# Optimization experiments

Measured on AMD Instinct MI355X. Metric: run time of the kernel, lower is better.

Reference implementation:

```python
import jax, jax.numpy as jnp
import numpy as np

D_STATE = 16
LOW_RANK = 6


def _scan_fwd(t):
    # 'interwave' scan: (B, stream, signal, C, H, W) -> (stream, B, C, H*W*signal)
    st, B, C = t.shape[1], t.shape[0], t.shape[3]
    t = jnp.transpose(t, (1, 0, 3, 4, 5, 2))  # stream,B,C,H,W,signal
    return t.reshape(st, B, C, -1)


def _scan_bwd(t, sg, H, W):
    # inverse 'interwave': (stream, B, C, H*W*sg) -> (B, stream, sg, C, H, W)
    st, B, C, _ = t.shape
    t = t.reshape(st, B, C, H, W, sg)
    return jnp.transpose(t, (1, 0, 5, 2, 3, 4))


def _layernorm(t, w, b):
    # LayerNorm over last (channel) axis, eps=1e-5 (torch default)
    mu = t.mean(-1, keepdims=True)
    var = t.var(-1, keepdims=True)
    return (t - mu) * jax.lax.rsqrt(var + 1e-5) * w + b


def reference(x, x_proj_weight, dt_projs_weight, dt_projs_bias, A_logs, Ds, norm_weight, norm_bias):
    B, S, C, H, W = x.shape
    stream = S + 1
    G = 4 * stream            # scan_direction * stream groups
    N = D_STATE
    R = LOW_RANK
    L = S * H * W             # unistream_length
    i = jnp.arange(S - 1)
    j = jnp.arange(S)

    # ---- CommDiffSS2DScan (cross-scan) ----
    x_comm_0 = _scan_fwd(x[:, None])                                  # (1,B,C,L)
    x_comm_1 = _scan_fwd(jnp.swapaxes(x, -1, -2)[:, None])
    x_dif = x[:, :, None] - x[:, None, :]                             # (B,S,S,C,H,W)
    x_dif = x_dif.at[:, i, i].set(x_dif[:, i, S - 1])
    x_dif = x_dif.at[:, :, S - 1].set(x)
    x_diff_0 = _scan_fwd(x_dif)                                       # (S,B,C,L)
    x_diff_1 = _scan_fwd(jnp.swapaxes(x_dif, -1, -2))
    xs0 = jnp.concatenate([x_diff_0, x_comm_0], 0)                    # (stream,B,C,L)
    xs1 = jnp.concatenate([x_diff_1, x_comm_1], 0)
    xs = jnp.stack([xs0, xs1, xs0[..., ::-1], xs1[..., ::-1]], 0)     # (4,stream,B,C,L)
    xs = jnp.transpose(xs, (2, 0, 1, 3, 4))                           # (B,4,stream,C,L)

    # ---- input-dependent projections ----
    x_dbl = jnp.einsum('bkscl,kspc->bkspl', xs, x_proj_weight)        # (B,4,stream,R+2N,L)
    dts, Bs, Cs = jnp.split(x_dbl, [R, R + N], axis=3)
    dts = jnp.einsum('bksrl,kscr->bkscl', dts, dt_projs_weight)       # (B,4,stream,C,L)

    u = xs.reshape(B, G, C, L)
    delta = jax.nn.softplus(dts.reshape(B, G, C, L) + dt_projs_bias.reshape(G, C)[None, :, :, None])
    A = -jnp.exp(A_logs).reshape(G, C, N)
    Bm = Bs.reshape(B, G, N, L)
    Cm = Cs.reshape(B, G, N, L)

    # ---- selective scan along L ----
    def step(h, inp):
        u_, d_, b_, c_ = inp                                          # (B,G,C),(B,G,C),(B,G,N),(B,G,N)
        h = h * jnp.exp(d_[..., None] * A) + (d_ * u_)[..., None] * b_[:, :, None, :]
        return h, jnp.einsum('bgcn,bgn->bgc', h, c_)

    h0 = jnp.zeros((B, G, C, N), x.dtype)
    _, ys = jax.lax.scan(step, h0, (jnp.moveaxis(u, -1, 0), jnp.moveaxis(delta, -1, 0),
                                    jnp.moveaxis(Bm, -1, 0), jnp.moveaxis(Cm, -1, 0)))
    ys = jnp.moveaxis(ys, 0, -1) + Ds.reshape(G, C)[None, :, :, None] * u  # (B,G,C,L)

    # ---- CommDiffSS2DMerge (cross-merge) ----
    ys = jnp.transpose(ys.reshape(B, 4, stream, C, L), (1, 2, 0, 3, 4))   # (4,stream,B,C,L)
    ys = ys[:2] + ys[2:, ..., ::-1]                                       # (2,stream,B,C,L)
    yd = _scan_bwd(ys[0, :S], S, H, W) + jnp.swapaxes(_scan_bwd(ys[1, :S], S, W, H), -1, -2)
    y = yd[:, :, S - 1]
    yd = yd.at[:, i, S - 1].set(yd[:, i, i])
    yd = yd.at[:, j, j].set(0.0)
    y_dif_extend = yd.sum(2)
    y_com = (_scan_bwd(ys[0, S:], S, H, W) + jnp.swapaxes(_scan_bwd(ys[1, S:], S, W, H), -1, -2)).reshape(B, S, C, H, W)

    tocl = lambda t: jnp.transpose(t, (0, 1, 3, 4, 2))  # channels-last for out_norm
    return (_layernorm(tocl(y), norm_weight, norm_bias),
            _layernorm(tocl(y_com), norm_weight, norm_bias),
            _layernorm(tocl(y_dif_extend), norm_weight, norm_bias))


def setup_inputs() -> dict:
    key = jax.random.key(0)
    ks = jax.random.split(key, 6)
    B, S, C, H, W = 4, 2, 96, 32, 32
    stream = S + 1
    G = 4 * stream
    N, R = D_STATE, LOW_RANK
    P = N + N + R
    return {
        'x': jax.random.normal(ks[0], (B, S, C, H, W), jnp.float32),
        'x_proj_weight': jax.random.normal(ks[1], (4, stream, P, C), jnp.float32) * 0.1,
        'dt_projs_weight': jax.random.normal(ks[2], (4, stream, C, R), jnp.float32) * 0.1,
        'dt_projs_bias': jax.random.uniform(ks[3], (G * C,), jnp.float32) * 0.1,
        'A_logs': jax.random.uniform(ks[4], (G * C, N), jnp.float32),
        'Ds': jax.random.normal(ks[5], (G * C,), jnp.float32) * 0.1,
        'norm_weight': jnp.ones((C,), jnp.float32),
        'norm_bias': jnp.zeros((C,), jnp.float32),
    }
```

## Files before the change

### kernel.cpp

```cpp
#include <hip/hip_runtime.h>
#include <math.h>

typedef float f4 __attribute__((ext_vector_type(4)));
typedef float f2 __attribute__((ext_vector_type(2)));

#define L_LEN 2048
#define C_DIM 96
#define N_DIM 16
#define R_DIM 6
#define G_DIM 12
#define B_DIM 4
#define NCHUNK 64
#define CLEN 32
#define BGC (B_DIM * G_DIM * C_DIM)

#define SZ_DELTA (B_DIM * G_DIM * L_LEN * C_DIM)
#define SZ_BC (B_DIM * G_DIM * N_DIM * L_LEN)
#define SZ_U6 (B_DIM * 6 * C_DIM * L_LEN)
#define SZ_Y (B_DIM * G_DIM * C_DIM * L_LEN)
#define SZ_H (BGC * NCHUNK * N_DIM)
#define SZ_S (BGC * NCHUNK)
#define SZ_X (B_DIM * 2 * C_DIM * 1024)
#define SZ_WPAD (G_DIM * 40 * C_DIM)

__device__ __forceinline__ float fexp2(float x) { return __builtin_amdgcn_exp2f(x); }

__device__ __forceinline__ float softplus_f(float x)
{
    float sp = __logf(1.f + __expf(x));
    return (x > 20.f) ? x : sp;
}

__global__ __launch_bounds__(256) void k0_xT(
    const float* __restrict__ x, float* __restrict__ xT)
{
    __shared__ float t[32][33];
    int img = blockIdx.x;
    const float* src = x + (size_t)img * 1024;
    float* dst = xT + (size_t)img * 1024;
    int tx = threadIdx.x & 31, ty = threadIdx.x >> 5;
#pragma unroll
    for (int r = 0; r < 32; r += 8) t[ty + r][tx] = src[(ty + r) * 32 + tx];
    __syncthreads();
#pragma unroll
    for (int r = 0; r < 32; r += 8) dst[(ty + r) * 32 + tx] = t[tx][ty + r];
}

__global__ __launch_bounds__(256) void k0b_padw(
    const float* __restrict__ xpw, float* __restrict__ wpad)
{
    int i = blockIdx.x * 256 + (int)threadIdx.x;
    if (i >= G_DIM * 40 * C_DIM) return;
    int g = i / (40 * C_DIM);
    int rem = i - g * 40 * C_DIM;
    int p = rem / C_DIM, c = rem - (rem / C_DIM) * C_DIM;
    wpad[i] = (p < 38) ? xpw[((size_t)g * 38 + p) * C_DIM + c] : 0.f;
}

__global__ __launch_bounds__(256) void k1_proj(
    const float* __restrict__ x, const float* __restrict__ xT,
    const float* __restrict__ wpad, const float* __restrict__ dtw,
    const float* __restrict__ dtb,
    float* __restrict__ deltaT, float* __restrict__ Bsw,
    float* __restrict__ Csw, float* __restrict__ u6T)
{
    __shared__ float Vsh[C_DIM * 68];
    __shared__ float Psh[40][68];

    int blk = blockIdx.x;
    int ltile = blk & 31;
    int bks = blk >> 5;
    int s = bks % 3;
    int k = (bks / 3) & 1;
    int b = bks / 6;
    int g = k * 3 + s;
    int gh = g + 6;
    int l0 = ltile * 64;
    int l0h = (31 - ltile) * 64;
    int bg = b * G_DIM + g;
    int bgh = b * G_DIM + gh;
    int tid = (int)threadIdx.x;

    const float* xb = (k ? xT : x) + (size_t)b * 2 * C_DIM * 1024;

#pragma unroll
    for (int j = 0; j < 6; ++j) {
        int e = tid + j * 256;
        int c = e >> 4;
        int llq = (e & 15) * 4;
        int pp = (l0 + llq) >> 1;
        f2 x0 = *(const f2*)(xb + (size_t)c * 1024 + pp);
        f2 x1 = *(const f2*)(xb + (size_t)(C_DIM + c) * 1024 + pp);
        f4 v;
        if (s == 2)      { v[0] = x0.x; v[1] = x1.x; v[2] = x0.y; v[3] = x1.y; }
        else if (s == 1) { v[0] = x1.x - x0.x; v[1] = x1.x; v[2] = x1.y - x0.y; v[3] = x1.y; }
        else             { v[0] = x0.x - x1.x; v[1] = x0.x; v[2] = x0.y - x1.y; v[3] = x0.y; }
        *(f4*)(Vsh + c * 68 + llq) = v;
    }
    __syncthreads();

    {
        size_t ub = ((size_t)(b * 6 + g) * L_LEN + l0) * C_DIM;
#pragma unroll
        for (int j = 0; j < 6; ++j) {
            int e = tid + j * 256;
            int lidx = e / 24;
            int c4 = (e - lidx * 24) * 4;
            f4 v = { Vsh[(c4 + 0) * 68 + lidx], Vsh[(c4 + 1) * 68 + lidx],
                     Vsh[(c4 + 2) * 68 + lidx], Vsh[(c4 + 3) * 68 + lidx] };
            *(f4*)(u6T + ub + (size_t)lidx * C_DIM + c4) = v;
        }
    }

    int ll = tid & 63;
    int P0 = __builtin_amdgcn_readfirstlane((tid >> 6) * 10);
    const float* wp = wpad + (size_t)g * 3840 + (size_t)P0 * C_DIM;
    const float* wph = wpad + (size_t)gh * 3840 + (size_t)P0 * C_DIM;

    float acc[10], acch[10];
#pragma unroll
    for (int p = 0; p < 10; ++p) { acc[p] = 0.f; acch[p] = 0.f; }

    for (int cb = 0; cb < C_DIM; cb += 8) {
        float vc[8], vch[8];
#pragma unroll
        for (int i = 0; i < 8; ++i) {
            vc[i] = Vsh[(cb + i) * 68 + ll];
            vch[i] = Vsh[(cb + i) * 68 + 63 - ll];
        }
#pragma unroll
        for (int p = 0; p < 10; ++p) {
#pragma unroll
            for (int q = 0; q < 2; ++q) {
                f4 w = *(const f4*)(wp + p * C_DIM + cb + q * 4);
                f4 wh = *(const f4*)(wph + p * C_DIM + cb + q * 4);
#pragma unroll
                for (int i = 0; i < 4; ++i) {
                    acc[p] = fmaf(w[i], vc[q * 4 + i], acc[p]);
                    acch[p] = fmaf(wh[i], vch[q * 4 + i], acch[p]);
                }
            }
        }
    }

#pragma unroll
    for (int gg = 0; gg < 2; ++gg) {
        __syncthreads();
#pragma unroll
        for (int p = 0; p < 10; ++p) Psh[P0 + p][ll] = gg ? acch[p] : acc[p];
        __syncthreads();
        int lb = gg ? l0h : l0;
        int bgx = gg ? bgh : bg;
        int gx = gg ? gh : g;
        int q = tid & 3, lx = tid >> 2;
        f4 bv = { Psh[6 + q * 4 + 0][lx], Psh[6 + q * 4 + 1][lx],
                  Psh[6 + q * 4 + 2][lx], Psh[6 + q * 4 + 3][lx] };
        *(f4*)(Bsw + ((size_t)bgx * L_LEN + lb + lx) * N_DIM + q * 4) = bv;
        f4 cv = { Psh[22 + q * 4 + 0][lx], Psh[22 + q * 4 + 1][lx],
                  Psh[22 + q * 4 + 2][lx], Psh[22 + q * 4 + 3][lx] };
        *(f4*)(Csw + ((size_t)bgx * L_LEN + lb + lx) * N_DIM + q * 4) = cv;

        const float* wdg = dtw + (size_t)gx * C_DIM * R_DIM;
        const float* biasg = dtb + gx * C_DIM;
        size_t db = ((size_t)bgx * L_LEN + lb) * C_DIM;
        for (int e = tid; e < 64 * C_DIM; e += 256) {
            int lidx = e / 96, c = e - (e / 96) * 96;
            float dsum = biasg[c];
#pragma unroll
            for (int r = 0; r < R_DIM; ++r) dsum = fmaf(Psh[r][lidx], wdg[c * R_DIM + r], dsum);
            deltaT[db + (size_t)lidx * C_DIM + c] = softplus_f(dsum);
        }
    }
}

__global__ __launch_bounds__(192) void k2_scanA(
    const float* __restrict__ deltaT, const float* __restrict__ Bsw,
    const float* __restrict__ u6T, const float* __restrict__ A_logs,
    float* __restrict__ hend, float* __restrict__ Sbuf)
{
    __shared__ f4 Bsh[256];
    int blk = blockIdx.x;
    int chgrp = blk & 31;
    int bg = blk >> 5;
    int g = bg % G_DIM;
    int b = bg / G_DIM;
    int tid = (int)threadIdx.x;

    const f4* Bg = (const f4*)(Bsw + ((size_t)bg * L_LEN + chgrp * 64) * N_DIM);
    for (int i = tid; i < 256; i += 192) Bsh[i] = Bg[i];
    __syncthreads();

    int chl = tid / 96;
    int c = tid % 96;
    int ch = chgrp * 2 + chl;
    int bgc = bg * C_DIM + c;
    const bool rev = (g >= 6);
    int gu = rev ? (g - 6) : g;

    float a2[N_DIM];
    {
        const f4* Ap = (const f4*)(A_logs + ((size_t)g * C_DIM + c) * N_DIM);
        f4 Av[4] = { Ap[0], Ap[1], Ap[2], Ap[3] };
#pragma unroll
        for (int n = 0; n < N_DIM; ++n)
            a2[n] = -__expf(Av[n >> 2][n & 3]) * 1.44269504f;
    }

    const int LOFF = ch * CLEN;
    const float* dp = deltaT + ((size_t)bg * L_LEN + LOFF) * C_DIM + c;
    const float* up;
    int us;
    if (rev) { up = u6T + ((size_t)(b * 6 + gu) * L_LEN + (2047 - LOFF)) * C_DIM + c; us = -C_DIM; }
    else     { up = u6T + ((size_t)(b * 6 + gu) * L_LEN + LOFF) * C_DIM + c; us = C_DIM; }

    float h[N_DIM];
#pragma unroll
    for (int n = 0; n < N_DIM; ++n) h[n] = 0.f;
    float S = 0.f;

    float dbuf[4], ubuf[4];
#pragma unroll
    for (int j = 0; j < 4; ++j) { dbuf[j] = dp[j * C_DIM]; ubuf[j] = up[j * us]; }

    for (int jj = 0; jj < CLEN; jj += 4) {
        int nx = (jj + 4 < CLEN) ? jj + 4 : jj;
        float dn[4], un[4];
#pragma unroll
        for (int j = 0; j < 4; ++j) { dn[j] = dp[(nx + j) * C_DIM]; un[j] = up[(nx + j) * us]; }
#pragma unroll
        for (int j = 0; j < 4; ++j) {
            int li = chl * CLEN + jj + j;
            float d = dbuf[j];
            S += d;
            float du = d * ubuf[j];
            const f4* Bl = Bsh + (size_t)li * 4;
            f4 Bv[4] = { Bl[0], Bl[1], Bl[2], Bl[3] };
#pragma unroll
            for (int n = 0; n < N_DIM; ++n) {
                float e = fexp2(d * a2[n]);
                h[n] = fmaf(h[n], e, du * Bv[n >> 2][n & 3]);
            }
        }
#pragma unroll
        for (int j = 0; j < 4; ++j) { dbuf[j] = dn[j]; ubuf[j] = un[j]; }
    }
    float* hp = hend + ((size_t)bgc * NCHUNK + ch) * N_DIM;
#pragma unroll
    for (int q = 0; q < 4; ++q) {
        f4 hv = { h[q * 4], h[q * 4 + 1], h[q * 4 + 2], h[q * 4 + 3] };
        *(f4*)(hp + q * 4) = hv;
    }
    Sbuf[(size_t)bgc * NCHUNK + ch] = S;
}

__global__ __launch_bounds__(256) void k2_fix(
    const float* __restrict__ Sbuf, const float* __restrict__ A_logs, float* hh)
{
    int t = blockIdx.x * 256 + (int)threadIdx.x;
    int n = t & 15;
    int bgc = t >> 4;
    int c = bgc % C_DIM;
    int g = (bgc / C_DIM) % G_DIM;
    float a2 = -__expf(A_logs[((size_t)g * C_DIM + c) * N_DIM + n]) * 1.44269504f;
    const float* Sp = Sbuf + (size_t)bgc * NCHUNK;
    float h = 0.f;
    for (int ch = 0; ch < NCHUNK; ++ch) {
        size_t idx = ((size_t)bgc * NCHUNK + ch) * N_DIM + n;
        float he = hh[idx];
        float P = fexp2(a2 * Sp[ch]);
        hh[idx] = h;
        h = fmaf(h, P, he);
    }
}

__global__ __launch_bounds__(192) void k2_scanC(
    const float* __restrict__ deltaT, const float* __restrict__ Bsw,
    const float* __restrict__ Csw, const float* __restrict__ u6T,
    const float* __restrict__ A_logs, const float* __restrict__ Ds,
    const float* __restrict__ hstart, float* __restrict__ yssT)
{
    __shared__ f4 Bsh[256];
    __shared__ f4 Csh[256];
    int blk = blockIdx.x;
    int chgrp = blk & 31;
    int bg = blk >> 5;
    int g = bg % G_DIM;
    int b = bg / G_DIM;
    int tid = (int)threadIdx.x;

    const f4* Bg = (const f4*)(Bsw + ((size_t)bg * L_LEN + chgrp * 64) * N_DIM);
    const f4* Cg = (const f4*)(Csw + ((size_t)bg * L_LEN + chgrp * 64) * N_DIM);
    for (int i = tid; i < 256; i += 192) { Bsh[i] = Bg[i]; Csh[i] = Cg[i]; }
    __syncthreads();

    int chl = tid / 96;
    int c = tid % 96;
    int ch = chgrp * 2 + chl;
    int bgc = bg * C_DIM + c;
    const bool rev = (g >= 6);
    int gu = rev ? (g - 6) : g;

    float a2[N_DIM];
    {
        const f4* Ap = (const f4*)(A_logs + ((size_t)g * C_DIM + c) * N_DIM);
        f4 Av[4] = { Ap[0], Ap[1], Ap[2], Ap[3] };
#pragma unroll
        for (int n = 0; n < N_DIM; ++n)
            a2[n] = -__expf(Av[n >> 2][n & 3]) * 1.44269504f;
    }
    float dsc = Ds[g * C_DIM + c];

    const int LOFF = ch * CLEN;
    const float* dp = deltaT + ((size_t)bg * L_LEN + LOFF) * C_DIM + c;
    const float* up;
    int us;
    if (rev) { up = u6T + ((size_t)(b * 6 + gu) * L_LEN + (2047 - LOFF)) * C_DIM + c; us = -C_DIM; }
    else     { up = u6T + ((size_t)(b * 6 + gu) * L_LEN + LOFF) * C_DIM + c; us = C_DIM; }
    float* yp = yssT + ((size_t)bg * L_LEN + LOFF) * C_DIM + c;

    float h[N_DIM];
    {
        const f4* Hp = (const f4*)(hstart + ((size_t)bgc * NCHUNK + ch) * N_DIM);
        f4 Hv[4] = { Hp[0], Hp[1], Hp[2], Hp[3] };
#pragma unroll
        for (int n = 0; n < N_DIM; ++n) h[n] = Hv[n >> 2][n & 3];
    }

    float dbuf[4], ubuf[4];
#pragma unroll
    for (int j = 0; j < 4; ++j) { dbuf[j] = dp[j * C_DIM]; ubuf[j] = up[j * us]; }

    for (int jj = 0; jj < CLEN; jj += 4) {
        int nx = (jj + 4 < CLEN) ? jj + 4 : jj;
        float dn[4], un[4];
#pragma unroll
        for (int j = 0; j < 4; ++j) { dn[j] = dp[(nx + j) * C_DIM]; un[j] = up[(nx + j) * us]; }
#pragma unroll
        for (int j = 0; j < 4; ++j) {
            int li = chl * CLEN + jj + j;
            float d = dbuf[j];
            float uu = ubuf[j];
            float du = d * uu;
            const f4* Bl = Bsh + (size_t)li * 4;
            const f4* Cl = Csh + (size_t)li * 4;
            f4 Bv[4] = { Bl[0], Bl[1], Bl[2], Bl[3] };
            f4 Cv[4] = { Cl[0], Cl[1], Cl[2], Cl[3] };
            float y0 = dsc * uu, y1 = 0.f, y2 = 0.f, y3 = 0.f;
#pragma unroll
            for (int q = 0; q < 4; ++q) {
                float e0 = fexp2(d * a2[q * 4 + 0]);
                float e1 = fexp2(d * a2[q * 4 + 1]);
                float e2 = fexp2(d * a2[q * 4 + 2]);
                float e3 = fexp2(d * a2[q * 4 + 3]);
                h[q * 4 + 0] = fmaf(h[q * 4 + 0], e0, du * Bv[q][0]);
                h[q * 4 + 1] = fmaf(h[q * 4 + 1], e1, du * Bv[q][1]);
                h[q * 4 + 2] = fmaf(h[q * 4 + 2], e2, du * Bv[q][2]);
                h[q * 4 + 3] = fmaf(h[q * 4 + 3], e3, du * Bv[q][3]);
                y0 = fmaf(h[q * 4 + 0], Cv[q][0], y0);
                y1 = fmaf(h[q * 4 + 1], Cv[q][1], y1);
                y2 = fmaf(h[q * 4 + 2], Cv[q][2], y2);
                y3 = fmaf(h[q * 4 + 3], Cv[q][3], y3);
            }
            yp[(jj + j) * C_DIM] = (y0 + y1) + (y2 + y3);
        }
#pragma unroll
        for (int j = 0; j < 4; ++j) { dbuf[j] = dn[j]; ubuf[j] = un[j]; }
    }
}

__global__ __launch_bounds__(256) void k3_out(
    const float* __restrict__ yssT, const float* __restrict__ nw,
    const float* __restrict__ nb, float* __restrict__ out)
{
    __shared__ float tA[32][97];
    __shared__ float tB[32][97];
    __shared__ float ps[4][8][32];
    __shared__ float stat[4][32];

    int blk = blockIdx.x;
    int h = blk & 31;
    int bs = blk >> 5;
    int so = bs & 1;
    int b = bs >> 1;
    int tid = (int)threadIdx.x;

    auto Y = [&](int g) { return yssT + (size_t)(b * 12 + g) * L_LEN * C_DIM; };
    const float* Y0 = Y(so);
    const float* Y0r = Y(6 + so);
    const float* Y1 = Y(3 + so);
    const float* Y1r = Y(9 + so);

#pragma unroll 2
    for (int it = 0; it < 24; ++it) {
        int idx = tid + it * 256;
        int c = idx % 96, rest = idx / 96;
        int w = rest >> 1, par = rest & 1;
        int a0 = h * 64 + rest;
        int a1 = w * 64 + 2 * h + par;
        float v = Y0[(size_t)a0 * C_DIM + c] + Y0r[(size_t)(2047 - a0) * C_DIM + c]
                + Y1[(size_t)a1 * C_DIM + c] + Y1r[(size_t)(2047 - a1) * C_DIM + c];
        if (par) tA[w][c] = v; else tB[w][c] = v;
    }
    __syncthreads();

    int w = tid & 31, cg = tid >> 5;
    float sA = 0, qA = 0, sB = 0, qB = 0;
#pragma unroll
    for (int j = 0; j < 12; ++j) {
        float yv = tA[w][cg * 12 + j], dv = tB[w][cg * 12 + j];
        sA += yv; qA += yv * yv; sB += dv; qB += dv * dv;
    }
    ps[0][cg][w] = sA; ps[1][cg][w] = qA; ps[2][cg][w] = sB; ps[3][cg][w] = qB;
    __syncthreads();
    if (tid < 32) {
        int ww = tid;
        float t0 = 0, t1 = 0, t2 = 0, t3 = 0;
#pragma unroll
        for (int q = 0; q < 8; ++q) {
            t0 += ps[0][q][ww]; t1 += ps[1][q][ww];
            t2 += ps[2][q][ww]; t3 += ps[3][q][ww];
        }
        float muA = t0 * (1.f / 96.f), eqA = t1 * (1.f / 96.f);
        float muB = t2 * (1.f / 96.f), eqB = t3 * (1.f / 96.f);
        stat[0][ww] = muA; stat[1][ww] = rsqrtf(eqA - muA * muA + 1e-5f);
        stat[2][ww] = muB; stat[3][ww] = rsqrtf(eqB - muB * muB + 1e-5f);
    }
    __syncthreads();
    size_t obase = (size_t)blk * 3072;
    for (int e = tid; e < 3072; e += 256) {
        int ww = e / 96, c = e % 96;
        float wc = nw[c], bc = nb[c];
        out[obase + e] = (tA[ww][c] - stat[0][ww]) * stat[1][ww] * wc + bc;
        out[2 * 786432 + obase + e] = (tB[ww][c] - stat[2][ww]) * stat[3][ww] * wc + bc;
    }
    __syncthreads();

    const float* Y2 = Y(2);
    const float* Y2r = Y(8);
    const float* Y3 = Y(5);
    const float* Y3r = Y(11);
#pragma unroll 2
    for (int it = 0; it < 12; ++it) {
        int idx = tid + it * 256;
        int c = idx % 96, w2 = idx / 96;
        int a0 = h * 64 + 2 * w2 + so;
        int a1 = w2 * 64 + 2 * h + so;
        float v = Y2[(size_t)a0 * C_DIM + c] + Y2r[(size_t)(2047 - a0) * C_DIM + c]
                + Y3[(size_t)a1 * C_DIM + c] + Y3r[(size_t)(2047 - a1) * C_DIM + c];
        tA[w2][c] = v;
    }
    __syncthreads();
    float sC = 0, qC = 0;
#pragma unroll
    for (int j = 0; j < 12; ++j) {
        float v = tA[w][cg * 12 + j];
        sC += v; qC += v * v;
    }
    ps[0][cg][w] = sC; ps[1][cg][w] = qC;
    __syncthreads();
    if (tid < 32) {
        int ww = tid;
        float t0 = 0, t1 = 0;
#pragma unroll
        for (int q = 0; q < 8; ++q) { t0 += ps[0][q][ww]; t1 += ps[1][q][ww]; }
        float mu = t0 * (1.f / 96.f), eq = t1 * (1.f / 96.f);
        stat[0][ww] = mu; stat[1][ww] = rsqrtf(eq - mu * mu + 1e-5f);
    }
    __syncthreads();
    for (int e = tid; e < 3072; e += 256) {
        int ww = e / 96, c = e % 96;
        out[786432 + obase + e] = (tA[ww][c] - stat[0][ww]) * stat[1][ww] * nw[c] + nb[c];
    }
}

extern "C" void kernel_launch(void* const* d_in, const int* in_sizes, int n_in,
                              void* d_out, int out_size, void* d_ws, size_t ws_size,
                              hipStream_t stream)
{
    const float* x = (const float*)d_in[0];
    const float* xpw = (const float*)d_in[1];
    const float* dtw = (const float*)d_in[2];
    const float* dtb = (const float*)d_in[3];
    const float* A_logs = (const float*)d_in[4];
    const float* Ds = (const float*)d_in[5];
    const float* nw = (const float*)d_in[6];
    const float* nb = (const float*)d_in[7];
    float* out = (float*)d_out;

    float* ws = (float*)d_ws;
    float* deltaT = ws;
    float* Bsw = deltaT + SZ_DELTA;
    float* Csw = Bsw + SZ_BC;
    float* u6T = Csw + SZ_BC;
    float* yssT = u6T + SZ_U6;
    float* xT = yssT;
    float* wpad = yssT + SZ_X;
    float* hend = yssT + SZ_Y;
    float* Sbuf = hend + SZ_H;

    k0_xT<<<dim3(768), dim3(256), 0, stream>>>(x, xT);
    k0b_padw<<<dim3(180), dim3(256), 0, stream>>>(xpw, wpad);
    k1_proj<<<dim3(24 * 32), dim3(256), 0, stream>>>(x, xT, wpad, dtw, dtb, deltaT, Bsw, Csw, u6T);
    k2_scanA<<<dim3(48 * 32), dim3(192), 0, stream>>>(deltaT, Bsw, u6T, A_logs, hend, Sbuf);
    k2_fix<<<dim3(288), dim3(256), 0, stream>>>(Sbuf, A_logs, hend);
    k2_scanC<<<dim3(48 * 32), dim3(192), 0, stream>>>(deltaT, Bsw, Csw, u6T, A_logs, Ds, hend, yssT);
    k3_out<<<dim3(256), dim3(256), 0, stream>>>(yssT, nw, nb, out);
}
```

Measured before the change: 150.1 us.

## Process two channels per thread with packed f2 math in chunked scans

Each thread in the two chunked selective-scan kernels now handles a pair of adjacent channels using float2 vectors and packed FMA, and each block covers four chunks (a 128-step window) instead of two, which halves the grid. The aim is to use packed FP32 FMA instructions, issue wider f2 loads and stores for delta, u and y, and share the B/C shared-memory reads across two channels. In exchange each thread keeps twice as many state registers and there are half as many blocks, which can lower occupancy and parallelism. The exp2 calls stay scalar, so they are not packed.

Result: slower. 158.2 us (+5.4%).

```diff
diff --git a/kernel.cpp b/kernel.cpp
--- a/kernel.cpp
+++ b/kernel.cpp
@@ -12,6 +12,7 @@
 #define B_DIM 4
 #define NCHUNK 64
 #define CLEN 32
+#define WINL 128
 #define BGC (B_DIM * G_DIM * C_DIM)
 
 #define SZ_DELTA (B_DIM * G_DIM * L_LEN * C_DIM)
@@ -24,6 +25,7 @@
 #define SZ_WPAD (G_DIM * 40 * C_DIM)
 
 __device__ __forceinline__ float fexp2(float x) { return __builtin_amdgcn_exp2f(x); }
+__device__ __forceinline__ f2 pkfma(f2 a, f2 b, f2 c) { return __builtin_elementwise_fma(a, b, c); }
 
 __device__ __forceinline__ float softplus_f(float x)
 {
@@ -178,79 +180,92 @@
     const float* __restrict__ u6T, const float* __restrict__ A_logs,
     float* __restrict__ hend, float* __restrict__ Sbuf)
 {
-    __shared__ f4 Bsh[256];
+    __shared__ f4 Bsh[512];
     int blk = blockIdx.x;
-    int chgrp = blk & 31;
-    int bg = blk >> 5;
+    int win = blk & 15;
+    int bg = blk >> 4;
     int g = bg % G_DIM;
     int b = bg / G_DIM;
     int tid = (int)threadIdx.x;
 
-    const f4* Bg = (const f4*)(Bsw + ((size_t)bg * L_LEN + chgrp * 64) * N_DIM);
-    for (int i = tid; i < 256; i += 192) Bsh[i] = Bg[i];
-    __syncthreads();
-
-    int chl = tid / 96;
-    int c = tid % 96;
-    int ch = chgrp * 2 + chl;
-    int bgc = bg * C_DIM + c;
+    const f4* Bg = (const f4*)(Bsw + ((size_t)bg * L_LEN + win * WINL) * N_DIM);
+    for (int i = tid; i < 512; i += 192) Bsh[i] = Bg[i];
+    __syncthreads();
+
+    int chl = tid / 48;
+    int cp = tid % 48;
+    int c0 = cp * 2;
+    int ch = win * 4 + chl;
     const bool rev = (g >= 6);
     int gu = rev ? (g - 6) : g;
 
-    float a2[N_DIM];
+    f2 a2[N_DIM];
     {
-        const f4* Ap = (const f4*)(A_logs + ((size_t)g * C_DIM + c) * N_DIM);
-        f4 Av[4] = { Ap[0], Ap[1], Ap[2], Ap[3] };
-#pragma unroll
-        for (int n = 0; n < N_DIM; ++n)
-            a2[n] = -__expf(Av[n >> 2][n & 3]) * 1.44269504f;
+        const f4* A0 = (const f4*)(A_logs + ((size_t)g * C_DIM + c0) * N_DIM);
+        const f4* A1 = (const f4*)(A_logs + ((size_t)g * C_DIM + c0 + 1) * N_DIM);
+#pragma unroll
+        for (int q = 0; q < 4; ++q) {
+            f4 v0 = A0[q], v1 = A1[q];
+#pragma unroll
+            for (int i = 0; i < 4; ++i)
+                a2[q * 4 + i] = (f2){ -__expf(v0[i]) * 1.44269504f, -__expf(v1[i]) * 1.44269504f };
+        }
     }
 
     const int LOFF = ch * CLEN;
-    const float* dp = deltaT + ((size_t)bg * L_LEN + LOFF) * C_DIM + c;
+    const float* dp = deltaT + ((size_t)bg * L_LEN + LOFF) * C_DIM + c0;
     const float* up;
     int us;
-    if (rev) { up = u6T + ((size_t)(b * 6 + gu) * L_LEN + (2047 - LOFF)) * C_DIM + c; us = -C_DIM; }
-    else     { up = u6T + ((size_t)(b * 6 + gu) * L_LEN + LOFF) * C_DIM + c; us = C_DIM; }
-
-    float h[N_DIM];
-#pragma unroll
-    for (int n = 0; n < N_DIM; ++n) h[n] = 0.f;
-    float S = 0.f;
-
-    float dbuf[4], ubuf[4];
-#pragma unroll
-    for (int j = 0; j < 4; ++j) { dbuf[j] = dp[j * C_DIM]; ubuf[j] = up[j * us]; }
-
-    for (int jj = 0; jj < CLEN; jj += 4) {
-        int nx = (jj + 4 < CLEN) ? jj + 4 : jj;
-        float dn[4], un[4];
-#pragma unroll
-        for (int j = 0; j < 4; ++j) { dn[j] = dp[(nx + j) * C_DIM]; un[j] = up[(nx + j) * us]; }
-#pragma unroll
-        for (int j = 0; j < 4; ++j) {
+    if (rev) { up = u6T + ((size_t)(b * 6 + gu) * L_LEN + (2047 - LOFF)) * C_DIM + c0; us = -C_DIM; }
+    else     { up = u6T + ((size_t)(b * 6 + gu) * L_LEN + LOFF) * C_DIM + c0; us = C_DIM; }
+
+    f2 h2[N_DIM];
+#pragma unroll
+    for (int n = 0; n < N_DIM; ++n) h2[n] = (f2){0.f, 0.f};
+    f2 S2 = {0.f, 0.f};
+
+    f2 dbuf[2], ubuf[2];
+#pragma unroll
+    for (int j = 0; j < 2; ++j) { dbuf[j] = *(const f2*)(dp + j * C_DIM); ubuf[j] = *(const f2*)(up + j * us); }
+
+    for (int jj = 0; jj < CLEN; jj += 2) {
+        int nx = (jj + 2 < CLEN) ? jj + 2 : jj;
+        f2 dn[2], un[2];
+#pragma unroll
+        for (int j = 0; j < 2; ++j) { dn[j] = *(const f2*)(dp + (nx + j) * C_DIM); un[j] = *(const f2*)(up + (nx + j) * us); }
+#pragma unroll
+        for (int j = 0; j < 2; ++j) {
             int li = chl * CLEN + jj + j;
-            float d = dbuf[j];
-            S += d;
-            float du = d * ubuf[j];
+            f2 dv = dbuf[j];
+            S2 += dv;
+            f2 du2 = dv * ubuf[j];
             const f4* Bl = Bsh + (size_t)li * 4;
-            f4 Bv[4] = { Bl[0], Bl[1], Bl[2], Bl[3] };
-#pragma unroll
-            for (int n = 0; n < N_DIM; ++n) {
-                float e = fexp2(d * a2[n]);
-                h[n] = fmaf(h[n], e, du * Bv[n >> 2][n & 3]);
+#pragma unroll
+            for (int q = 0; q < 4; ++q) {
+                f4 Bq = Bl[q];
+#pragma unroll
+                for (int i = 0; i < 4; ++i) {
+                    int n = q * 4 + i;
+                    f2 m = dv * a2[n];
+                    f2 e = { fexp2(m.x), fexp2(m.y) };
+                    h2[n] = pkfma(h2[n], e, du2 * (f2){Bq[i], Bq[i]});
+                }
             }
         }
 #pragma unroll
-        for (int j = 0; j < 4; ++j) { dbuf[j] = dn[j]; ubuf[j] = un[j]; }
-    }
-    float* hp = hend + ((size_t)bgc * NCHUNK + ch) * N_DIM;
+        for (int j = 0; j < 2; ++j) { dbuf[j] = dn[j]; ubuf[j] = un[j]; }
+    }
+    size_t base0 = ((size_t)(bg * C_DIM + c0) * NCHUNK + ch) * N_DIM;
+    size_t base1 = base0 + (size_t)NCHUNK * N_DIM;
 #pragma unroll
     for (int q = 0; q < 4; ++q) {
-        f4 hv = { h[q * 4], h[q * 4 + 1], h[q * 4 + 2], h[q * 4 + 3] };
-        *(f4*)(hp + q * 4) = hv;
-    }
-    Sbuf[(size_t)bgc * NCHUNK + ch] = S;
+        f4 h0 = { h2[q * 4].x, h2[q * 4 + 1].x, h2[q * 4 + 2].x, h2[q * 4 + 3].x };
+        f4 h1 = { h2[q * 4].y, h2[q * 4 + 1].y, h2[q * 4 + 2].y, h2[q * 4 + 3].y };
+        *(f4*)(hend + base0 + q * 4) = h0;
+        *(f4*)(hend + base1 + q * 4) = h1;
+    }
+    Sbuf[(size_t)(bg * C_DIM + c0) * NCHUNK + ch] = S2.x;
+    Sbuf[(size_t)(bg * C_DIM + c0 + 1) * NCHUNK + ch] = S2.y;
 }
 
 __global__ __launch_bounds__(256) void k2_fix(
@@ -279,92 +294,114 @@
     const float* __restrict__ A_logs, const float* __restrict__ Ds,
     const float* __restrict__ hstart, float* __restrict__ yssT)
 {
-    __shared__ f4 Bsh[256];
-    __shared__ f4 Csh[256];
+    __shared__ f4 Bsh[512];
+    __shared__ f4 Csh[512];
     int blk = blockIdx.x;
-    int chgrp = blk & 31;
-    int bg = blk >> 5;
+    int win = blk & 15;
+    int bg = blk >> 4;
     int g = bg % G_DIM;
     int b = bg / G_DIM;
     int tid = (int)threadIdx.x;
 
-    const f4* Bg = (const f4*)(Bsw + ((size_t)bg * L_LEN + chgrp * 64) * N_DIM);
-    const f4* Cg = (const f4*)(Csw + ((size_t)bg * L_LEN + chgrp * 64) * N_DIM);
-    for (int i = tid; i < 256; i += 192) { Bsh[i] = Bg[i]; Csh[i] = Cg[i]; }
-    __syncthreads();
-
-    int chl = tid / 96;
-    int c = tid % 96;
-    int ch = chgrp * 2 + chl;
-    int bgc = bg * C_DIM + c;
+    const f4* Bg = (const f4*)(Bsw + ((size_t)bg * L_LEN + win * WINL) * N_DIM);
+    const f4* Cg = (const f4*)(Csw + ((size_t)bg * L_LEN + win * WINL) * N_DIM);
+    for (int i = tid; i < 512; i += 192) { Bsh[i] = Bg[i]; Csh[i] = Cg[i]; }
+    __syncthreads();
+
+    int chl = tid / 48;
+    int cp = tid % 48;
+    int c0 = cp * 2;
+    int ch = win * 4 + chl;
     const bool rev = (g >= 6);
     int gu = rev ? (g - 6) : g;
 
-    float a2[N_DIM];
+    f2 a2[N_DIM];
     {
-        const f4* Ap = (const f4*)(A_logs + ((size_t)g * C_DIM + c) * N_DIM);
-        f4 Av[4] = { Ap[0], Ap[1], Ap[2], Ap[3] };
-#pragma unroll
-        for (int n = 0; n < N_DIM; ++n)
-            a2[n] = -__expf(Av[n >> 2][n & 3]) * 1.44269504f;
-    }
-    float dsc = Ds[g * C_DIM + c];
+        const f4* A0 = (const f4*)(A_logs + ((size_t)g * C_DIM + c0) * N_DIM);
+        const f4* A1 = (const f4*)(A_logs + ((size_t)g * C_DIM + c0 + 1) * N_DIM);
+#pragma unroll
+        for (int q = 0; q < 4; ++q) {
+            f4 v0 = A0[q], v1 = A1[q];
+#pragma unroll
+            for (int i = 0; i < 4; ++i)
+                a2[q * 4 + i] = (f2){ -__expf(v0[i]) * 1.44269504f, -__expf(v1[i]) * 1.44269504f };
+        }
+    }
+    f2 dsc = *(const f2*)(Ds + g * C_DIM + c0);
 
     const int LOFF = ch * CLEN;
-    const float* dp = deltaT + ((size_t)bg * L_LEN + LOFF) * C_DIM + c;
+    const float* dp = deltaT + ((size_t)bg * L_LEN + LOFF) * C_DIM + c0;
     const float* up;
     int us;
-    if (rev) { up = u6T + ((size_t)(b * 6 + gu) * L_LEN + (2047 - LOFF)) * C_DIM + c; us = -C_DIM; }
-    else     { up = u6T + ((size_t)(b * 6 + gu) * L_LEN + LOFF) * C_DIM + c; us = C_DIM; }
-    float* yp = yssT + ((size_t)bg * L_LEN + LOFF) * C_DIM + c;
-
-    float h[N_DIM];
+    if (rev) { up = u6T + ((size_t)(b * 6 + gu) * L_LEN + (2047 - LOFF)) * C_DIM + c0; us = -C_DIM; }
+    else     { up = u6T + ((size_t)(b * 6 + gu) * L_LEN + LOFF) * C_DIM + c0; us = C_DIM; }
+    float* yp = yssT + ((size_t)bg * L_LEN + LOFF) * C_DIM + c0;
+
+    f2 h2[N_DIM];
     {
-        const f4* Hp = (const f4*)(hstart + ((size_t)bgc * NCHUNK + ch) * N_DIM);
-        f4 Hv[4] = { Hp[0], Hp[1], Hp[2], Hp[3] };
-#pragma unroll
-        for (int n = 0; n < N_DIM; ++n) h[n] = Hv[n >> 2][n & 3];
-    }
-
-    float dbuf[4], ubuf[4];
-#pragma unroll
-    for (int j = 0; j < 4; ++j) { dbuf[j] = dp[j * C_DIM]; ubuf[j] = up[j * us]; }
-
-    for (int jj = 0; jj < CLEN; jj += 4) {
-        int nx = (jj + 4 < CLEN) ? jj + 4 : jj;
-        float dn[4], un[4];
-#pragma unroll
-        for (int j = 0; j < 4; ++j) { dn[j] = dp[(nx + j) * C_DIM]; un[j] = up[(nx + j) * us]; }
-#pragma unroll
-        for (int j = 0; j < 4; ++j) {
+        size_t base0 = ((size_t)(bg * C_DIM + c0) * NCHUNK + ch) * N_DIM;
+        size_t base1 = base0 + (size_t)NCHUNK * N_DIM;
+#pragma unroll
+        for (int q = 0; q < 4; ++q) {
+            f4 h0 = *(const f4*)(hstart + base0 + q * 4);
+            f4 h1 = *(const f4*)(hstart + base1 + q * 4);
+#pragma unroll
+            for (int i = 0; i < 4; ++i) h2[q * 4 + i] = (f2){ h0[i], h1[i] };
+        }
+    }
+
+    f2 dbuf[2], ubuf[2];
+#pragma unroll
+    for (int j = 0; j < 2; ++j) { dbuf[j] = *(const f2*)(dp + j * C_DIM); ubuf[j] = *(const f2*)(up + j * us); }
+
+    for (int jj = 0; jj < CLEN; jj += 2) {
+        int nx = (jj + 2 < CLEN) ? jj + 2 : jj;
+        f2 dn[2], un[2];
+#pragma unroll
+        for (int j = 0; j < 2; ++j) { dn[j] = *(const f2*)(dp + (nx + j) * C_DIM); un[j] = *(const f2*)(up + (nx + j) * us); }
+#pragma unroll
+        for (int j = 0; j < 2; ++j) {
             int li = chl * CLEN + jj + j;
-            float d = dbuf[j];
-            float uu = ubuf[j];
-            float du = d * uu;
+            f2 dv = dbuf[j];
+            f2 uv = ubuf[j];
+            f2 du2 = dv * uv;
             const f4* Bl = Bsh + (size_t)li * 4;
             const f4* Cl = Csh + (size_t)li * 4;
-            f4 Bv[4] = { Bl[0], Bl[1], Bl[2], Bl[3] };
-            f4 Cv[4] = { Cl[0], Cl[1], Cl[2], Cl[3] };
-            float y0 = dsc * uu, y1 = 0.f, y2 = 0.f, y3 = 0.f;
+            f2 ya = dsc * uv, yb = {0.f, 0.f}, yc = {0.f, 0.f}, yd = {0.f, 0.f};
 #pragma unroll
             for (int q = 0; q < 4; ++q) {
-                float e0 = fexp2(d * a2[q * 4 + 0]);
-                float e1 = fexp2(d * a2[q * 4 + 1]);
-                float e2 = fexp2(d * a2[q * 4 + 2]);
-                float e3 = fexp2(d * a2[q * 4 + 3]);
-                h[q * 4 + 0] = fmaf(h[q * 4 + 0], e0, du * Bv[q][0]);
-                h[q * 4 + 1] = fmaf(h[q * 4 + 1], e1, du * Bv[q][1]);
-                h[q * 4 + 2] = fmaf(h[q * 4 + 2], e2, du * Bv[q][2]);
-                h[q * 4 + 3] = fmaf(h[q * 4 + 3], e3, du * Bv[q][3]);
-                y0 = fmaf(h[q * 4 + 0], Cv[q][0], y0);
-                y1 = fmaf(h[q * 4 + 1], Cv[q][1], y1);
-                y2 = fmaf(h[q * 4 + 2], Cv[q][2], y2);
-                y3 = fmaf(h[q * 4 + 3], Cv[q][3], y3);
+                f4 Bq = Bl[q];
+                f4 Cq = Cl[q];
+                {
+                    f2 m = dv * a2[q * 4 + 0];
+                    f2 e = { fexp2(m.x), fexp2(m.y) };
+                    h2[q * 4 + 0] = pkfma(h2[q * 4 + 0], e, du2 * (f2){Bq[0], Bq[0]});
+                    ya = pkfma(h2[q * 4 + 0], (f2){Cq[0], Cq[0]}, ya);
+                }
+                {
+                    f2 m = dv * a2[q * 4 + 1];
+                    f2 e = { fexp2(m.x), fexp2(m.y) };
+                    h2[q * 4 + 1] = pkfma(h2[q * 4 + 1], e, du2 * (f2){Bq[1], Bq[1]});
+                    yb = pkfma(h2[q * 4 + 1], (f2){Cq[1], Cq[1]}, yb);
+                }
+                {
+                    f2 m = dv * a2[q * 4 + 2];
+                    f2 e = { fexp2(m.x), fexp2(m.y) };
+                    h2[q * 4 + 2] = pkfma(h2[q * 4 + 2], e, du2 * (f2){Bq[2], Bq[2]});
+                    yc = pkfma(h2[q * 4 + 2], (f2){Cq[2], Cq[2]}, yc);
+                }
+                {
+                    f2 m = dv * a2[q * 4 + 3];
+                    f2 e = { fexp2(m.x), fexp2(m.y) };
+                    h2[q * 4 + 3] = pkfma(h2[q * 4 + 3], e, du2 * (f2){Bq[3], Bq[3]});
+                    yd = pkfma(h2[q * 4 + 3], (f2){Cq[3], Cq[3]}, yd);
+                }
             }
-            yp[(jj + j) * C_DIM] = (y0 + y1) + (y2 + y3);
-        }
-#pragma unroll
-        for (int j = 0; j < 4; ++j) { dbuf[j] = dn[j]; ubuf[j] = un[j]; }
+            f2 yv = (ya + yb) + (yc + yd);
+            *(f2*)(yp + (jj + j) * C_DIM) = yv;
+        }
+#pragma unroll
+        for (int j = 0; j < 2; ++j) { dbuf[j] = dn[j]; ubuf[j] = un[j]; }
     }
 }
 
@@ -501,8 +538,8 @@
     k0_xT<<<dim3(768), dim3(256), 0, stream>>>(x, xT);
     k0b_padw<<<dim3(180), dim3(256), 0, stream>>>(xpw, wpad);
     k1_proj<<<dim3(24 * 32), dim3(256), 0, stream>>>(x, xT, wpad, dtw, dtb, deltaT, Bsw, Csw, u6T);
-    k2_scanA<<<dim3(48 * 32), dim3(192), 0, stream>>>(deltaT, Bsw, u6T, A_logs, hend, Sbuf);
+    k2_scanA<<<dim3(48 * 16), dim3(192), 0, stream>>>(deltaT, Bsw, u6T, A_logs, hend, Sbuf);
     k2_fix<<<dim3(288), dim3(256), 0, stream>>>(Sbuf, A_logs, hend);
-    k2_scanC<<<dim3(48 * 32), dim3(192), 0, stream>>>(deltaT, Bsw, Csw, u6T, A_logs, Ds, hend, yssT);
+    k2_scanC<<<dim3(48 * 16), dim3(192), 0, stream>>>(deltaT, Bsw, Csw, u6T, A_logs, Ds, hend, yssT);
     k3_out<<<dim3(256), dim3(256), 0, stream>>>(yssT, nw, nb, out);
 }
```

## Split projection kernel per direction group to double block count

Applied to the files above, without the earlier changes.

The projection kernel previously had each block compute both a forward group and its reversed counterpart. Now every one of the 12 groups gets its own block, and reversed groups load their inputs at mirrored positions. This doubles the grid to 1536 blocks and halves per-thread accumulator registers, aiming at better occupancy and latency hiding. The cost is loading and staging the input tile twice. The Psh padding also changes from 68 to 65 to reduce LDS bank conflicts.

Result: faster. 133.2 us (-11.3%).

```diff
diff --git a/kernel.cpp b/kernel.cpp
--- a/kernel.cpp
+++ b/kernel.cpp
@@ -65,20 +65,18 @@
     float* __restrict__ Csw, float* __restrict__ u6T)
 {
     __shared__ float Vsh[C_DIM * 68];
-    __shared__ float Psh[40][68];
+    __shared__ float Psh[40][65];
 
     int blk = blockIdx.x;
     int ltile = blk & 31;
     int bks = blk >> 5;
-    int s = bks % 3;
-    int k = (bks / 3) & 1;
-    int b = bks / 6;
-    int g = k * 3 + s;
-    int gh = g + 6;
+    int g = bks % G_DIM;
+    int b = bks / G_DIM;
+    const bool rev = (g >= 6);
+    int gu = rev ? (g - 6) : g;
+    int k = gu / 3, s = gu % 3;
     int l0 = ltile * 64;
-    int l0h = (31 - ltile) * 64;
     int bg = b * G_DIM + g;
-    int bgh = b * G_DIM + gh;
     int tid = (int)threadIdx.x;
 
     const float* xb = (k ? xT : x) + (size_t)b * 2 * C_DIM * 1024;
@@ -88,18 +86,24 @@
         int e = tid + j * 256;
         int c = e >> 4;
         int llq = (e & 15) * 4;
-        int pp = (l0 + llq) >> 1;
+        int pp = rev ? (1022 - ((l0 + llq) >> 1)) : ((l0 + llq) >> 1);
         f2 x0 = *(const f2*)(xb + (size_t)c * 1024 + pp);
         f2 x1 = *(const f2*)(xb + (size_t)(C_DIM + c) * 1024 + pp);
         f4 v;
-        if (s == 2)      { v[0] = x0.x; v[1] = x1.x; v[2] = x0.y; v[3] = x1.y; }
-        else if (s == 1) { v[0] = x1.x - x0.x; v[1] = x1.x; v[2] = x1.y - x0.y; v[3] = x1.y; }
-        else             { v[0] = x0.x - x1.x; v[1] = x0.x; v[2] = x0.y - x1.y; v[3] = x0.y; }
+        if (!rev) {
+            if (s == 2)      { v[0] = x0.x; v[1] = x1.x; v[2] = x0.y; v[3] = x1.y; }
+            else if (s == 1) { v[0] = x1.x - x0.x; v[1] = x1.x; v[2] = x1.y - x0.y; v[3] = x1.y; }
+            else             { v[0] = x0.x - x1.x; v[1] = x0.x; v[2] = x0.y - x1.y; v[3] = x0.y; }
+        } else {
+            if (s == 2)      { v[0] = x1.y; v[1] = x0.y; v[2] = x1.x; v[3] = x0.x; }
+            else if (s == 1) { v[0] = x1.y; v[1] = x1.y - x0.y; v[2] = x1.x; v[3] = x1.x - x0.x; }
+            else             { v[0] = x0.y; v[1] = x0.y - x1.y; v[2] = x0.x; v[3] = x0.x - x1.x; }
+        }
         *(f4*)(Vsh + c * 68 + llq) = v;
     }
     __syncthreads();
 
-    {
+    if (!rev) {
         size_t ub = ((size_t)(b * 6 + g) * L_LEN + l0) * C_DIM;
 #pragma unroll
         for (int j = 0; j < 6; ++j) {
@@ -115,61 +119,51 @@
     int ll = tid & 63;
     int P0 = __builtin_amdgcn_readfirstlane((tid >> 6) * 10);
     const float* wp = wpad + (size_t)g * 3840 + (size_t)P0 * C_DIM;
-    const float* wph = wpad + (size_t)gh * 3840 + (size_t)P0 * C_DIM;
-
-    float acc[10], acch[10];
-#pragma unroll
-    for (int p = 0; p < 10; ++p) { acc[p] = 0.f; acch[p] = 0.f; }
+
+    float acc[10];
+#pragma unroll
+    for (int p = 0; p < 10; ++p) acc[p] = 0.f;
 
     for (int cb = 0; cb < C_DIM; cb += 8) {
-        float vc[8], vch[8];
-#pragma unroll
-        for (int i = 0; i < 8; ++i) {
-            vc[i] = Vsh[(cb + i) * 68 + ll];
-            vch[i] = Vsh[(cb + i) * 68 + 63 - ll];
-        }
+        float vc[8];
+#pragma unroll
+        for (int i = 0; i < 8; ++i) vc[i] = Vsh[(cb + i) * 68 + ll];
 #pragma unroll
         for (int p = 0; p < 10; ++p) {
 #pragma unroll
             for (int q = 0; q < 2; ++q) {
                 f4 w = *(const f4*)(wp + p * C_DIM + cb + q * 4);
-                f4 wh = *(const f4*)(wph + p * C_DIM + cb + q * 4);
-#pragma unroll
-                for (int i = 0; i < 4; ++i) {
+#pragma unroll
+                for (int i = 0; i < 4; ++i)
                     acc[p] = fmaf(w[i], vc[q * 4 + i], acc[p]);
-                    acch[p] = fmaf(wh[i], vch[q * 4 + i], acch[p]);
-                }
             }
         }
     }
 
-#pragma unroll
-    for (int gg = 0; gg < 2; ++gg) {
-        __syncthreads();
-#pragma unroll
-        for (int p = 0; p < 10; ++p) Psh[P0 + p][ll] = gg ? acch[p] : acc[p];
-        __syncthreads();
-        int lb = gg ? l0h : l0;
-        int bgx = gg ? bgh : bg;
-        int gx = gg ? gh : g;
+    __syncthreads();
+#pragma unroll
+    for (int p = 0; p < 10; ++p) Psh[P0 + p][ll] = acc[p];
+    __syncthreads();
+    {
         int q = tid & 3, lx = tid >> 2;
         f4 bv = { Psh[6 + q * 4 + 0][lx], Psh[6 + q * 4 + 1][lx],
                   Psh[6 + q * 4 + 2][lx], Psh[6 + q * 4 + 3][lx] };
-        *(f4*)(Bsw + ((size_t)bgx * L_LEN + lb + lx) * N_DIM + q * 4) = bv;
+        *(f4*)(Bsw + ((size_t)bg * L_LEN + l0 + lx) * N_DIM + q * 4) = bv;
         f4 cv = { Psh[22 + q * 4 + 0][lx], Psh[22 + q * 4 + 1][lx],
                   Psh[22 + q * 4 + 2][lx], Psh[22 + q * 4 + 3][lx] };
-        *(f4*)(Csw + ((size_t)bgx * L_LEN + lb + lx) * N_DIM + q * 4) = cv;
-
-        const float* wdg = dtw + (size_t)gx * C_DIM * R_DIM;
-        const float* biasg = dtb + gx * C_DIM;
-        size_t db = ((size_t)bgx * L_LEN + lb) * C_DIM;
-        for (int e = tid; e < 64 * C_DIM; e += 256) {
-            int lidx = e / 96, c = e - (e / 96) * 96;
-            float dsum = biasg[c];
-#pragma unroll
-            for (int r = 0; r < R_DIM; ++r) dsum = fmaf(Psh[r][lidx], wdg[c * R_DIM + r], dsum);
-            deltaT[db + (size_t)lidx * C_DIM + c] = softplus_f(dsum);
-        }
+        *(f4*)(Csw + ((size_t)bg * L_LEN + l0 + lx) * N_DIM + q * 4) = cv;
+    }
+    const float* wdg = dtw + (size_t)g * C_DIM * R_DIM;
+    const float* biasg = dtb + g * C_DIM;
+    size_t db = ((size_t)bg * L_LEN + l0) * C_DIM;
+#pragma unroll
+    for (int it = 0; it < 24; ++it) {
+        int e = tid + it * 256;
+        int lidx = e / 96, c = e - (e / 96) * 96;
+        float dsum = biasg[c];
+#pragma unroll
+        for (int r = 0; r < R_DIM; ++r) dsum = fmaf(Psh[r][lidx], wdg[c * R_DIM + r], dsum);
+        deltaT[db + (size_t)lidx * C_DIM + c] = softplus_f(dsum);
     }
 }
 
@@ -500,7 +494,7 @@
 
     k0_xT<<<dim3(768), dim3(256), 0, stream>>>(x, xT);
     k0b_padw<<<dim3(180), dim3(256), 0, stream>>>(xpw, wpad);
-    k1_proj<<<dim3(24 * 32), dim3(256), 0, stream>>>(x, xT, wpad, dtw, dtb, deltaT, Bsw, Csw, u6T);
+    k1_proj<<<dim3(48 * 32), dim3(256), 0, stream>>>(x, xT, wpad, dtw, dtb, deltaT, Bsw, Csw, u6T);
     k2_scanA<<<dim3(48 * 32), dim3(192), 0, stream>>>(deltaT, Bsw, u6T, A_logs, hend, Sbuf);
     k2_fix<<<dim3(288), dim3(256), 0, stream>>>(Sbuf, A_logs, hend);
     k2_scanC<<<dim3(48 * 32), dim3(192), 0, stream>>>(deltaT, Bsw, Csw, u6T, A_logs, Ds, hend, yssT);
```
